# Optimization experiments

Measured on AMD Instinct MI355X. Metric: run time of the kernel, lower is better.

The kernel has to match this reference:

```python
import jax, jax.numpy as jnp
import numpy as np

B, T, D_MODEL, H, W = 2, 3, 32, 256, 256
N_HEADS, N_LEVELS, N_POINTS = 4, 3, 4


def conv2d(x, w, b, padding=1, dilation=1):
    y = jax.lax.conv_general_dilated(
        x, w, window_strides=(1, 1),
        padding=[(padding, padding), (padding, padding)],
        rhs_dilation=(dilation, dilation),
        dimension_numbers=('NCHW', 'OIHW', 'NCHW'))
    return y + b[None, :, None, None]


def lrelu(x):
    return jnp.where(x >= 0, x, 0.1 * x)


def bilinear_sample(img, x, y):
    # img: (N,C,H,W); x,y: (N,H',W') pixel coords; zero padding outside (grid_sample zeros)
    N, C, Hh, Ww = img.shape
    x0 = jnp.floor(x); y0 = jnp.floor(y)
    lx = x - x0; ly = y - y0
    imf = img.reshape(N, C, Hh * Ww)
    out = jnp.zeros((N, C) + x.shape[1:], img.dtype)
    for dy, dx, wgt in ((0, 0, (1 - lx) * (1 - ly)), (0, 1, lx * (1 - ly)),
                        (1, 0, (1 - lx) * ly), (1, 1, lx * ly)):
        xi = x0 + dx; yi = y0 + dy
        valid = (xi >= 0) & (xi < Ww) & (yi >= 0) & (yi < Hh)
        idx = (jnp.clip(yi, 0, Hh - 1) * Ww + jnp.clip(xi, 0, Ww - 1)).astype(jnp.int32)
        g = jnp.take_along_axis(imf, idx.reshape(N, 1, -1), axis=2).reshape((N, C) + x.shape[1:])
        out = out + g * (wgt * valid)[:, None]
    return out


def flow_warp(x, flow):
    # torch flow_warp with align_corners=True == sampling at pixel coords grid+flow
    N, C, Hh, Ww = x.shape
    gy, gx = jnp.meshgrid(jnp.arange(Hh, dtype=x.dtype), jnp.arange(Ww, dtype=x.dtype), indexing='ij')
    return bilinear_sample(x, gx[None] + flow[:, 0], gy[None] + flow[:, 1])


def ms_deform_attn(value, sampling_locations, attention_weights, h, w):
    # value: (N, L*h*w, Hh, d); loc: (N, Lq, Hh, L, P, 2) in [0,1]; weights: (N, Lq, Hh, L, P)
    # Matches MSDA CUDA kernel: sample at loc*(W,H)-0.5, bilinear, zero pad outside.
    N, _, Hh, d = value.shape
    Lq = sampling_locations.shape[1]
    L, P = sampling_locations.shape[3], sampling_locations.shape[4]
    out = jnp.zeros((N, Lq, Hh, d), value.dtype)
    for l in range(L):
        v = value[:, l * h * w:(l + 1) * h * w].transpose(0, 2, 1, 3)  # (N,Hh,hw,d)
        loc = sampling_locations[:, :, :, l]  # (N,Lq,Hh,P,2)
        x = loc[..., 0] * w - 0.5
        y = loc[..., 1] * h - 0.5
        x0 = jnp.floor(x); y0 = jnp.floor(y)
        lx = x - x0; ly = y - y0
        samp = jnp.zeros((N, Lq, Hh, P, d), value.dtype)
        for dy, dx, wgt in ((0, 0, (1 - lx) * (1 - ly)), (0, 1, lx * (1 - ly)),
                            (1, 0, (1 - lx) * ly), (1, 1, lx * ly)):
            xi = x0 + dx; yi = y0 + dy
            valid = (xi >= 0) & (xi < w) & (yi >= 0) & (yi < h)
            idx = (jnp.clip(yi, 0, h - 1) * w + jnp.clip(xi, 0, w - 1)).astype(jnp.int32)
            idx = idx.transpose(0, 2, 1, 3).reshape(N, Hh, Lq * P)
            g = jnp.take_along_axis(v, idx[..., None], axis=2)  # (N,Hh,Lq*P,d)
            g = g.reshape(N, Hh, Lq, P, d).transpose(0, 2, 1, 3, 4)
            samp = samp + g * (wgt * valid)[..., None]
        out = out + (samp * attention_weights[:, :, :, l][..., None]).sum(axis=3)
    return out.reshape(N, Lq, Hh * d)


def setup_inputs() -> dict:
    key = jax.random.key(0)
    ks = jax.random.split(key, 24)
    def rn(k, shape, s=1.0):
        return jax.random.normal(k, shape, dtype=jnp.float32) * s
    c = D_MODEL
    nofp = N_HEADS * N_LEVELS * N_POINTS
    return {
        'frame': rn(ks[0], (B, T, c, H, W)),
        'srcframe': rn(ks[1], (B, T, c, H, W)),
        'flow_forward': rn(ks[2], (B, T - 1, 2, H, W), 2.0),
        'flow_backward': rn(ks[3], (B, T - 1, 2, H, W), 2.0),
        'W_qk': rn(ks[4], (3 * c, 3 * c + 4, 3, 3), 0.05), 'b_qk': rn(ks[5], (3 * c,), 0.05),
        'W_v': rn(ks[6], (3 * c, 3 * c, 3, 3), 0.05), 'b_v': rn(ks[7], (3 * c,), 0.05),
        'W_vp': rn(ks[8], (c, c, 3, 3), 0.05), 'b_vp': rn(ks[9], (c,), 0.05),
        'W_off': rn(ks[10], (nofp * 2, 3 * c, 3, 3), 0.01), 'b_off': rn(ks[11], (nofp * 2,), 0.5),
        'W_aw': rn(ks[12], (nofp, 3 * c, 3, 3), 0.05), 'b_aw': rn(ks[13], (nofp,), 0.05),
        'W_out': rn(ks[14], (c, c, 3, 3), 0.05), 'b_out': rn(ks[15], (c,), 0.05),
        'W_ffd': rn(ks[16], (c, c, 3, 3), 0.05), 'b_ffd': rn(ks[17], (c,), 0.05),
        'W_ff1': rn(ks[18], (c, 2 * c, 3, 3), 0.05), 'b_ff1': rn(ks[19], (c,), 0.05),
        'W_ff2': rn(ks[20], (c, c, 3, 3), 0.05), 'b_ff2': rn(ks[21], (c,), 0.05),
        'W_fu': rn(ks[22], (c, c, 1, 1), 0.05), 'b_fu': rn(ks[23], (c,), 0.05),
    }


def reference(frame, srcframe, flow_forward, flow_backward,
              W_qk, b_qk, W_v, b_v, W_vp, b_vp, W_off, b_off, W_aw, b_aw,
              W_out, b_out, W_ffd, b_ffd, W_ff1, b_ff1, W_ff2, b_ff2, W_fu, b_fu):
    b, t, c, h, w = frame.shape
    Hh, L, P = N_HEADS, N_LEVELS, N_POINTS
    d = c // Hh
    # flow-warped neighbor frames + flows -> query embedding
    warp01 = flow_warp(frame[:, 0], flow_backward[:, 0])
    warp21 = flow_warp(frame[:, 2], flow_forward[:, 1])
    qk_in = jnp.concatenate([warp01, frame[:, 1], warp21,
                             flow_forward[:, 1], flow_backward[:, 0]], axis=1)
    qureys = lrelu(conv2d(qk_in, W_qk, b_qk))                       # (b, 3c, h, w)
    value = conv2d(frame.reshape(b, t * c, h, w), W_v, b_v)         # (b, 3c, h, w)
    # --- MSDeformAttn_Fusion ---
    val = conv2d(value.reshape(b * t, c, h, w), W_vp, b_vp).reshape(b, t, c, h, w)
    off = conv2d(qureys, W_off, b_off)                               # (b, Hh*L*P*2, h, w)
    aw = conv2d(qureys, W_aw, b_aw)                                  # (b, Hh*L*P, h, w)
    value_flat = val.reshape(b, t, c, h * w).transpose(0, 1, 3, 2).reshape(b, t * h * w, Hh, d)
    off = off.reshape(b, -1, h * w).transpose(0, 2, 1).reshape(b, h * w, Hh, L, P, 2)
    aw = aw.reshape(b, -1, h * w).transpose(0, 2, 1).reshape(b, h * w, Hh, L * P)
    aw = jax.nn.softmax(aw, axis=-1).reshape(b, h * w, Hh, L, P)
    # reference points: pixel centers normalized (masks all zero -> valid_ratios == 1)
    gy, gx = jnp.meshgrid((jnp.arange(h, dtype=off.dtype) + 0.5) / h,
                          (jnp.arange(w, dtype=off.dtype) + 0.5) / w, indexing='ij')
    ref = jnp.stack([gx.reshape(-1), gy.reshape(-1)], -1)            # (hw, 2) (x, y)
    normalizer = jnp.array([w, h], dtype=off.dtype)                  # same for all levels
    loc = ref[None, :, None, None, None, :] + off / normalizer
    attn_out = ms_deform_attn(value_flat, loc, aw, h, w)             # (b, hw, c)
    out = attn_out.reshape(b, h, w, c).transpose(0, 3, 1, 2)
    out = conv2d(out, W_out, b_out)                                  # output_proj
    # --- post-attention ---
    out = conv2d(out, W_ffd, b_ffd) + frame[:, 1]
    tseq = jnp.concatenate([out, srcframe[:, 1]], axis=1)            # (b, 2c, h, w)
    ff = conv2d(lrelu(conv2d(tseq, W_ff1, b_ff1, padding=2, dilation=2)), W_ff2, b_ff2)
    out = out + ff
    out = lrelu(conv2d(out, W_fu, b_fu, padding=0))                  # fusion 1x1
    return out
```

## Files before the change

kernel.cpp:

```cpp
#include <hip/hip_runtime.h>
#include <hip/hip_bf16.h>

typedef __hip_bfloat16 bf16;
typedef unsigned short us;
typedef unsigned int u32;
typedef __attribute__((ext_vector_type(8))) short short8;
typedef __attribute__((ext_vector_type(8))) unsigned short ushortx8;
typedef __attribute__((ext_vector_type(2))) float f32x2;
typedef __attribute__((ext_vector_type(4))) float f32x4;
typedef __attribute__((ext_vector_type(16))) float f32x16;

#define HW 65536
#define IMW 256
#define IMH 256

static __device__ __forceinline__ float u2f(us u) {
  return __uint_as_float(((unsigned)u) << 16);
}
static __device__ __forceinline__ us f2bu(float x) {
  bf16 h = __float2bfloat16(x);
  return *reinterpret_cast<us*>(&h);
}
static __device__ __forceinline__ unsigned pk2(float a, float b) {
  return (unsigned)f2bu(a) | ((unsigned)f2bu(b) << 16);
}

static __device__ __forceinline__ void gload_lds16(const void* g, void* l) {
  __builtin_amdgcn_global_load_lds(
      (const __attribute__((address_space(1))) u32*)g,
      (__attribute__((address_space(3))) u32*)l, 16, 0, 0);
}

struct PrepArgs {
  const float* src[9];
  us* dst[9];
  int OC[9], CIN[9], KPAD[9], LAY[9];
};

__global__ __launch_bounds__(256) void prep_weights(PrepArgs a) {
  int j = blockIdx.y;
  int n = blockIdx.x * 256 + threadIdx.x;
  int OC = a.OC[j], CIN = a.CIN[j], KPAD = a.KPAD[j];
  int tot = 9 * OC * KPAD;
  if (n >= tot) return;
  int oc, k;
  if (a.LAY[j] == 0) {
    int G = OC >> 4, NKC = KPAD >> 5;
    int e = n & 7;
    int m = (n >> 3) & 15;
    int q = (n >> 7) & 3;
    int rest = n >> 9;
    int kc = rest % NKC;
    int tg = rest / NKC;
    int g = tg % G;
    int t = tg / G;
    oc = g * 16 + m;
    k = kc * 32 + q * 8 + e;
    float v = (k < CIN) ? a.src[j][(size_t)(oc * CIN + k) * 9 + t] : 0.f;
    a.dst[j][n] = f2bu(v);
  } else {
    int OCT = OC >> 5, KH = KPAD >> 4;
    int e = n & 7;
    int l = (n >> 3) & 63;
    int rest = n >> 9;
    int jt = rest % OCT;
    int u = rest / OCT;
    int kh = u % KH;
    int t = u / KH;
    oc = jt * 32 + (l & 31);
    k = kh * 16 + (l >> 5) * 8 + e;
    float v = (k < CIN) ? a.src[j][(size_t)(oc * CIN + k) * 9 + t] : 0.f;
    a.dst[j][n] = f2bu(v);
  }
}

__global__ __launch_bounds__(256) void frame_to_nhwc(const float* __restrict__ frame,
                                                     unsigned* __restrict__ fn) {
  int pix = blockIdx.x * 256 + threadIdx.x;
  int b = blockIdx.y;
  const float* s = frame + (size_t)b * 96 * HW + pix;
  unsigned u[48];
#pragma unroll
  for (int j = 0; j < 48; ++j)
    u[j] = pk2(s[(size_t)(2 * j) * HW], s[(size_t)(2 * j + 1) * HW]);
  unsigned* d = fn + ((size_t)b * HW + pix) * 48;
#pragma unroll
  for (int j = 0; j < 12; ++j) {
    uint4 w;
    w.x = u[4 * j]; w.y = u[4 * j + 1]; w.z = u[4 * j + 2]; w.w = u[4 * j + 3];
    *(uint4*)&d[4 * j] = w;
  }
}

static __device__ void warp_nhwc(const us* __restrict__ fn, size_t bbase, int coff,
                                 float x, float y, unsigned* uo) {
  float x0f = floorf(x), y0f = floorf(y);
  float lx = x - x0f, ly = y - y0f;
  int x0 = (int)x0f, y0 = (int)y0f;
  float wt[4] = {(1.f - lx) * (1.f - ly), lx * (1.f - ly), (1.f - lx) * ly, lx * ly};
  float acc[32] = {};
#pragma unroll
  for (int k = 0; k < 4; ++k) {
    int xi = x0 + (k & 1), yi = y0 + (k >> 1);
    if ((unsigned)xi < IMW && (unsigned)yi < IMH) {
      const ushortx8* s =
          (const ushortx8*)(fn + (bbase + (size_t)yi * IMW + xi) * 96 + coff);
      float w = wt[k];
#pragma unroll
      for (int cj = 0; cj < 4; ++cj) {
        ushortx8 vv = s[cj];
#pragma unroll
        for (int e = 0; e < 8; ++e)
          acc[cj * 8 + e] = fmaf(w, u2f(vv[e]), acc[cj * 8 + e]);
      }
    }
  }
#pragma unroll
  for (int j = 0; j < 16; ++j) uo[j] = pk2(acc[2 * j], acc[2 * j + 1]);
}

__global__ __launch_bounds__(256) void build_qkin(
    const us* __restrict__ fn, const float* __restrict__ flowf,
    const float* __restrict__ flowb, unsigned* __restrict__ qk) {
  int pix = blockIdx.x * 256 + threadIdx.x;
  int b = blockIdx.y;
  int px = pix & 255, py = pix >> 8;

  float fbx = flowb[((size_t)(b * 2 + 0) * 2 + 0) * HW + pix];
  float fby = flowb[((size_t)(b * 2 + 0) * 2 + 1) * HW + pix];
  float ffx = flowf[((size_t)(b * 2 + 1) * 2 + 0) * HW + pix];
  float ffy = flowf[((size_t)(b * 2 + 1) * 2 + 1) * HW + pix];

  unsigned u[50];
  {
    const unsigned* s = (const unsigned*)(fn + ((size_t)b * HW + pix) * 96);
#pragma unroll
    for (int j = 0; j < 16; ++j) u[16 + j] = s[16 + j];
  }
  u[48] = pk2(ffx, ffy);
  u[49] = pk2(fbx, fby);

  warp_nhwc(fn, (size_t)b * HW, 0, (float)px + fbx, (float)py + fby, &u[0]);
  warp_nhwc(fn, (size_t)b * HW, 64, (float)px + ffx, (float)py + ffy, &u[32]);

  unsigned* qb = qk + ((size_t)b * HW + pix) * 50;
#pragma unroll
  for (int j = 0; j < 25; ++j) {
    uint2 t;
    t.x = u[2 * j];
    t.y = u[2 * j + 1];
    *(uint2*)(qb + 2 * j) = t;
  }
}

template <int CIN, int CST, int KPAD, int OCT, int KHC, bool LRELU>
__global__ __launch_bounds__(256) void conv3x3_m32(
    const us* __restrict__ in, const us* __restrict__ W2,
    const float* __restrict__ bias, us* __restrict__ out, int out_cst,
    int out_coff) {
  constexpr int COLS = 18, ROWS = 10, HALO = COLS * ROWS;
  constexpr int CIPAD = KPAD + 8;
  constexpr int CH = KPAD / 8;
  constexpr int KH = KPAD / 16;
  constexpr int SPT = KH / KHC;
  constexpr int NSTG = 9 * SPT;
  constexpr int CHB = KHC * OCT;
  __shared__ alignas(16) short lds[HALO * CIPAD];
  __shared__ alignas(16) short wlds[2][CHB * 512];

  const int z = blockIdx.z;
  const int px0 = blockIdx.x * 16, py0 = blockIdx.y * 8;
  const int lane = threadIdx.x & 63;
  const int wv = threadIdx.x >> 6;
  const int n = lane & 31;
  const int sr = n >> 4;
  const int colp = n & 15;
  const int kq = lane >> 5;

  f32x16 acc[OCT];
#pragma unroll
  for (int j = 0; j < OCT; ++j) acc[j] = 0.f;

  for (int c = threadIdx.x; c < HALO * CH; c += 256) {
    int p = c / CH, cb = c - p * CH;
    int row = p / COLS, col = p - row * COLS;
    int gy = py0 + row - 1, gx = px0 + col - 1;
    bool ok = ((unsigned)gy < IMH) && ((unsigned)gx < IMW);
    int ci0 = cb * 8;
    const us* gp = in + ((size_t)z * HW + (size_t)gy * IMW + gx) * CST + ci0;
    if (CIN == KPAD) {
      short8 v = (short8)0;
      if (ok) v = *(const short8*)gp;
      *(short8*)&lds[p * CIPAD + ci0] = v;
    } else {
      uint2 h0; h0.x = 0; h0.y = 0;
      uint2 h1; h1.x = 0; h1.y = 0;
      if (ok && ci0 + 4 <= CIN) h0 = *(const uint2*)gp;
      if (ok && ci0 + 8 <= CIN) h1 = *(const uint2*)(gp + 4);
      *(uint2*)&lds[p * CIPAD + ci0] = h0;
      *(uint2*)&lds[p * CIPAD + ci0 + 4] = h1;
    }
  }

#pragma unroll
  for (int r = 0; r < (CHB + 3) / 4; ++r) {
    int blk = r * 4 + wv;
    if (blk < CHB)
      gload_lds16(W2 + (size_t)(blk * 64 + lane) * 8, &wlds[0][blk * 512]);
  }
  __syncthreads();

  const int lanebase = ((wv * 2 + sr) * COLS + colp) * CIPAD + kq * 8;

  int buf = 0;
#pragma unroll 1
  for (int s = 0; s < NSTG; ++s) {
    if (s + 1 < NSTG) {
      const us* wn = W2 + (size_t)(s + 1) * (CHB * 512);
#pragma unroll
      for (int r = 0; r < (CHB + 3) / 4; ++r) {
        int blk = r * 4 + wv;
        if (blk < CHB)
          gload_lds16(wn + (size_t)(blk * 64 + lane) * 8,
                      &wlds[buf ^ 1][blk * 512]);
      }
    }
    const int t = s / SPT;
    const int kh0 = (s - t * SPT) * KHC;
    const int dy = t / 3 - 1, dx = t - (t / 3) * 3 - 1;
    const int sb = lanebase + ((dy + 1) * COLS + (dx + 1)) * CIPAD + kh0 * 16;
#pragma unroll
    for (int khr = 0; khr < KHC; ++khr) {
      short8 bf = *(const short8*)&lds[sb + khr * 16];
#pragma unroll
      for (int j = 0; j < OCT; ++j) {
        short8 af =
            *(const short8*)&wlds[buf][(khr * OCT + j) * 512 + lane * 8];
        acc[j] =
            __builtin_amdgcn_mfma_f32_32x32x16_bf16(af, bf, acc[j], 0, 0, 0);
      }
    }
    __syncthreads();
    buf ^= 1;
  }

  {
    int row = py0 + wv * 2 + sr;
    int pxc = px0 + colp;
    us* ob = out + ((size_t)z * HW + (size_t)row * IMW + pxc) * out_cst + out_coff;
#pragma unroll
    for (int j = 0; j < OCT; ++j) {
#pragma unroll
      for (int hi = 0; hi < 4; ++hi) {
        int oc0 = j * 32 + hi * 8 + kq * 4;
        f32x4 bb = *(const f32x4*)&bias[oc0];
        float v0 = acc[j][4 * hi + 0] + bb[0];
        float v1 = acc[j][4 * hi + 1] + bb[1];
        float v2 = acc[j][4 * hi + 2] + bb[2];
        float v3 = acc[j][4 * hi + 3] + bb[3];
        if (LRELU) {
          v0 = v0 >= 0.f ? v0 : 0.1f * v0;
          v1 = v1 >= 0.f ? v1 : 0.1f * v1;
          v2 = v2 >= 0.f ? v2 : 0.1f * v2;
          v3 = v3 >= 0.f ? v3 : 0.1f * v3;
        }
        uint2 w;
        w.x = pk2(v0, v1);
        w.y = pk2(v2, v3);
        *(uint2*)&ob[oc0] = w;
      }
    }
  }
}

template <int CIN, int CST, int KPAD, int DIL, int G, int ZDIV, int CSUB,
          int RES, int OUTMODE, bool LRELU>
__global__ __launch_bounds__(256) void conv3x3_mfma(
    const us* __restrict__ in, const us* __restrict__ W2,
    const float* __restrict__ bias, void* __restrict__ out, int out_cst,
    int out_coff, float* __restrict__ outB, const float* __restrict__ res,
    int res_cst, int res_coff) {
  constexpr int OC = G * 16;
  constexpr int COLS = 16 + 2 * DIL;
  constexpr int ROWS = 8 + 2 * DIL;
  constexpr int HALO = ROWS * COLS;
  constexpr int CIPAD = KPAD + 8;
  constexpr int CH = KPAD / 8;
  constexpr int NKC = KPAD / 32;
  constexpr int GW0 = (G + 1) / 2;
  constexpr int NU = 9 * NKC;
  __shared__ alignas(16) short lds[HALO * CIPAD];

  const int z = blockIdx.z;
  const int bin = z / ZDIV;
  const int coff = (z % ZDIV) * CSUB;
  const int px0 = blockIdx.x * 16, py0 = blockIdx.y * 8;
  const int lane = threadIdx.x & 63;
  const int wv = threadIdx.x >> 6;
  const int m = lane & 15, q = lane >> 4;
  const int gh = wv & 1, rh = wv >> 1;
  const int goff = gh * GW0;

  f32x4 acc[GW0][4];
#pragma unroll
  for (int g = 0; g < GW0; ++g)
#pragma unroll
    for (int r = 0; r < 4; ++r) acc[g][r] = 0.f;

  for (int c = threadIdx.x; c < HALO * CH; c += 256) {
    int p = c / CH, cb = c - p * CH;
    int row = p / COLS, col = p - row * COLS;
    int gy = py0 + row - DIL, gx = px0 + col - DIL;
    bool ok = ((unsigned)gy < IMH) && ((unsigned)gx < IMW);
    int ci0 = cb * 8;
    const us* gp = in + ((size_t)bin * HW + (size_t)gy * IMW + gx) * CST + coff + ci0;
    if (CIN == KPAD) {
      short8 v = (short8)0;
      if (ok) v = *(const short8*)gp;
      *(short8*)&lds[p * CIPAD + ci0] = v;
    } else {
      uint2 h0; h0.x = 0; h0.y = 0;
      uint2 h1; h1.x = 0; h1.y = 0;
      if (ok && ci0 + 4 <= CIN) h0 = *(const uint2*)gp;
      if (ok && ci0 + 8 <= CIN) h1 = *(const uint2*)(gp + 4);
      *(uint2*)&lds[p * CIPAD + ci0] = h0;
      *(uint2*)&lds[p * CIPAD + ci0 + 4] = h1;
    }
  }
  __syncthreads();

  const us* wl = W2 + (size_t)lane * 8;
  short8 af[2][GW0];
#pragma unroll
  for (int g = 0; g < GW0; ++g)
    if (goff + g < G)
      af[0][g] = *(const short8*)(wl + (size_t)((goff + g) * NKC) * 512);

#pragma unroll
  for (int u = 0; u < NU; ++u) {
    const int t = u / NKC, kc = u - t * NKC;
    if (u + 1 < NU) {
      const int t1 = (u + 1) / NKC, kc1 = (u + 1) - t1 * NKC;
#pragma unroll
      for (int g = 0; g < GW0; ++g)
        if (goff + g < G)
          af[(u + 1) & 1][g] =
              *(const short8*)(wl + (size_t)((t1 * G + goff + g) * NKC + kc1) * 512);
    }
    const int dy = t / 3 - 1, dx = t - (t / 3) * 3 - 1;
    short8 bfr[4];
#pragma unroll
    for (int r = 0; r < 4; ++r) {
      int rr = rh * 4 + r + DIL + dy * DIL;
      int cc = m + DIL + dx * DIL;
      bfr[r] = *(const short8*)&lds[(rr * COLS + cc) * CIPAD + kc * 32 + q * 8];
    }
#pragma unroll
    for (int g = 0; g < GW0; ++g)
      if (goff + g < G)
#pragma unroll
        for (int r = 0; r < 4; ++r)
          acc[g][r] = __builtin_amdgcn_mfma_f32_16x16x32_bf16(af[u & 1][g], bfr[r],
                                                              acc[g][r], 0, 0, 0);
  }

#pragma unroll
  for (int g = 0; g < GW0; ++g) {
    if (goff + g < G) {
      int oc0 = (goff + g) * 16 + q * 4;
      f32x4 bb = *(const f32x4*)&bias[oc0];
#pragma unroll
      for (int r = 0; r < 4; ++r) {
        int py = py0 + rh * 4 + r;
        int px = px0 + m;
        size_t pix = (size_t)py * IMW + px;
        f32x4 v;
#pragma unroll
        for (int e = 0; e < 4; ++e) {
          float x = acc[g][r][e] + bb[e];
          if (LRELU) x = x >= 0.f ? x : 0.1f * x;
          v[e] = x;
        }
        if (RES == 1) {
          f32x4 rv = *(const f32x4*)&res[((size_t)z * HW + pix) * res_cst + oc0];
#pragma unroll
          for (int e = 0; e < 4; ++e) v[e] += rv[e];
        }
        if (RES == 2) {
#pragma unroll
          for (int e = 0; e < 4; ++e)
            v[e] += res[((size_t)z * res_cst + res_coff + oc0 + e) * HW + pix];
        }
        if (OUTMODE == 0 || OUTMODE == 3) {
          uint2 w;
          w.x = pk2(v[0], v[1]);
          w.y = pk2(v[2], v[3]);
          *(uint2*)&((us*)out)[((size_t)z * HW + pix) * out_cst + out_coff + oc0] = w;
        }
        if (OUTMODE == 2)
          *(f32x4*)&((float*)out)[((size_t)z * HW + pix) * out_cst + oc0] = v;
        if (OUTMODE == 3)
          *(f32x4*)&outB[((size_t)z * HW + pix) * 32 + oc0] = v;
      }
    }
  }
}

__global__ __launch_bounds__(256) void deform_attn(
    const us* __restrict__ valp, const us* __restrict__ off,
    const float* __restrict__ aw, us* __restrict__ outp) {
  int tid = threadIdx.x;
  int half = tid & 1;
  int hh = (tid >> 1) & 3;
  int pix = blockIdx.x * 32 + (tid >> 3);
  int b = blockIdx.y;
  int px = pix & (IMW - 1), py = pix >> 8;

  us os[12];
  {
    const uint2* ob = (const uint2*)(off + ((size_t)b * HW + pix) * 96 +
                                     hh * 24 + half * 12);
    uint2 a0 = ob[0], a1 = ob[1], a2 = ob[2];
    *(uint2*)&os[0] = a0;
    *(uint2*)&os[4] = a1;
    *(uint2*)&os[8] = a2;
  }
  float wv[6];
  {
    const f32x2* ab = (const f32x2*)(aw + ((size_t)b * HW + pix) * 48 +
                                     hh * 12 + half * 6);
    f32x2 a0 = ab[0], a1 = ab[1], a2 = ab[2];
    wv[0] = a0.x; wv[1] = a0.y; wv[2] = a1.x;
    wv[3] = a1.y; wv[4] = a2.x; wv[5] = a2.y;
  }

  float m6 = wv[0];
#pragma unroll
  for (int i = 1; i < 6; ++i) m6 = fmaxf(m6, wv[i]);
  float mx = fmaxf(m6, __shfl_xor(m6, 1));
  float s6 = 0.f;
#pragma unroll
  for (int i = 0; i < 6; ++i) {
    wv[i] = __expf(wv[i] - mx);
    s6 += wv[i];
  }
  float inv = 1.f / (s6 + __shfl_xor(s6, 1));

  f32x2 acc2[4];
#pragma unroll
  for (int j = 0; j < 4; ++j) acc2[j] = 0.f;

#pragma unroll
  for (int i = 0; i < 6; ++i) {
    int pp = half * 6 + i;
    int l = pp >> 2;
    const us* vbase = valp + ((size_t)(b * 3 + l) * HW) * 32 + hh * 8;
    float x = (float)px + u2f(os[2 * i]);
    float y = (float)py + u2f(os[2 * i + 1]);
    float x0f = floorf(x), y0f = floorf(y);
    float lx = x - x0f, ly = y - y0f;
    int x0 = (int)x0f, y0 = (int)y0f;
    bool vx0 = (unsigned)x0 < IMW, vx1 = (unsigned)(x0 + 1) < IMW;
    bool vy0 = (unsigned)y0 < IMH, vy1 = (unsigned)(y0 + 1) < IMH;
    float a = wv[i] * inv;
    float ax0 = (1.f - lx) * a, ax1 = lx * a;
    float w00 = ax0 * (1.f - ly), w01 = ax1 * (1.f - ly);
    float w10 = ax0 * ly, w11 = ax1 * ly;
    const us* p00 = vbase + (size_t)((long)(y0 * IMW + x0)) * 32;
#pragma unroll
    for (int c = 0; c < 4; ++c) {
      bool ok = (c & 1 ? vx1 : vx0) && (c & 2 ? vy1 : vy0);
      float w = (c == 0) ? w00 : (c == 1) ? w01 : (c == 2) ? w10 : w11;
      const us* p = p00 + (c & 1) * 32 + (c >> 1) * (IMW * 32);
      if (ok) {
        uint4 uu = *(const uint4*)p;
        unsigned uarr[4] = {uu.x, uu.y, uu.z, uu.w};
#pragma unroll
        for (int j = 0; j < 4; ++j) {
          f32x2 v;
          v.x = __uint_as_float(uarr[j] << 16);
          v.y = __uint_as_float(uarr[j] & 0xffff0000u);
          acc2[j] += v * w;
        }
      }
    }
  }

  float accf[8];
#pragma unroll
  for (int j = 0; j < 4; ++j) {
    accf[2 * j] = acc2[j].x + __shfl_xor(acc2[j].x, 1);
    accf[2 * j + 1] = acc2[j].y + __shfl_xor(acc2[j].y, 1);
  }
  if (half == 0) {
    ushortx8 sv;
#pragma unroll
    for (int dd = 0; dd < 8; ++dd) sv[dd] = f2bu(accf[dd]);
    *(ushortx8*)(outp + ((size_t)b * HW + pix) * 32 + hh * 8) = sv;
  }
}

__global__ __launch_bounds__(256) void copy_src(const float* __restrict__ src,
                                                unsigned* __restrict__ out1b) {
  int pix = blockIdx.x * 256 + threadIdx.x;
  int b = blockIdx.y;
  const float* s = src + ((size_t)(b * 3 + 1) * 32) * HW + pix;
  unsigned u[16];
#pragma unroll
  for (int j = 0; j < 16; ++j)
    u[j] = pk2(s[(size_t)(2 * j) * HW], s[(size_t)(2 * j + 1) * HW]);
  unsigned* d = out1b + ((size_t)b * HW + pix) * 32 + 16;
#pragma unroll
  for (int j = 0; j < 4; ++j) {
    uint4 w;
    w.x = u[4 * j]; w.y = u[4 * j + 1]; w.z = u[4 * j + 2]; w.w = u[4 * j + 3];
    *(uint4*)&d[4 * j] = w;
  }
}

__global__ __launch_bounds__(256) void conv1x1_fu(
    const float* __restrict__ in, const float* __restrict__ wgt,
    const float* __restrict__ bias, float* __restrict__ out) {
  int pix = blockIdx.x * 256 + threadIdx.x;
  int b = blockIdx.y;
  float vin[32];
  {
    const f32x4* s = (const f32x4*)(in + ((size_t)b * HW + pix) * 32);
#pragma unroll
    for (int j = 0; j < 8; ++j) {
      f32x4 v = s[j];
#pragma unroll
      for (int e = 0; e < 4; ++e) vin[4 * j + e] = v[e];
    }
  }
#pragma unroll 1
  for (int oc = 0; oc < 32; ++oc) {
    float a = bias[oc];
#pragma unroll
    for (int ci = 0; ci < 32; ++ci) a = fmaf(wgt[oc * 32 + ci], vin[ci], a);
    a = a >= 0.f ? a : 0.1f * a;
    out[((size_t)b * 32 + oc) * HW + pix] = a;
  }
}

extern "C" void kernel_launch(void* const* d_in, const int* in_sizes, int n_in,
                              void* d_out, int out_size, void* d_ws, size_t ws_size,
                              hipStream_t stream) {
  (void)in_sizes; (void)n_in; (void)out_size;
  if (ws_size < 25614592ull * 4) return;

  const float* frame = (const float*)d_in[0];
  const float* srcframe = (const float*)d_in[1];
  const float* flowf = (const float*)d_in[2];
  const float* flowb = (const float*)d_in[3];

  float* ws = (float*)d_ws;
  us* wsu = (us*)d_ws;

  static const int w2off[9] = {0,      110592, 193536, 202752, 285696,
                               327168, 336384, 345600, 364032};
  us* fnhwc = (us*)(ws + 186624);
  unsigned* qk_u = (unsigned*)(ws + 6478080);
  us* qk = (us*)qk_u;
  us* Q = (us*)(ws + 13031680);
  us* V = (us*)(ws + 6478080);
  us* Vp = (us*)(ws + 19323136);
  us* offb = (us*)(ws + 186624);
  float* awb = (float*)(ws + 6478080);
  us* attn = (us*)(ws + 13031680);
  us* convout = (us*)(ws + 13031680 + 2097152);
  us* out1b = (us*)(ws + 6478080);
  unsigned* out1b_u = (unsigned*)out1b;
  float* out1f = (float*)(ws + 19323136);
  us* ff1out = (us*)(ws + 186624);
  float* out2 = (float*)(ws + 13031680);

  {
    PrepArgs pa;
    static const int srcidx[9] = {4, 6, 8, 10, 12, 14, 16, 18, 20};
    static const int OCs[9] = {96, 96, 32, 96, 48, 32, 32, 32, 32};
    static const int CINs[9] = {100, 96, 32, 96, 96, 32, 32, 64, 32};
    static const int KPADs[9] = {128, 96, 32, 96, 96, 32, 32, 64, 32};
    static const int LAYs[9] = {1, 1, 0, 1, 0, 0, 0, 0, 0};
    for (int i = 0; i < 9; ++i) {
      pa.src[i] = (const float*)d_in[srcidx[i]];
      pa.dst[i] = wsu + w2off[i];
      pa.OC[i] = OCs[i];
      pa.CIN[i] = CINs[i];
      pa.KPAD[i] = KPADs[i];
      pa.LAY[i] = LAYs[i];
    }
    prep_weights<<<dim3(432, 9), 256, 0, stream>>>(pa);
  }

  frame_to_nhwc<<<dim3(256, 2), 256, 0, stream>>>(frame, (unsigned*)fnhwc);

  build_qkin<<<dim3(256, 2), 256, 0, stream>>>(fnhwc, flowf, flowb, qk_u);

  dim3 cg2(16, 32, 2);

  conv3x3_m32<100, 100, 128, 3, 4, true><<<cg2, 256, 0, stream>>>(
      qk, wsu + w2off[0], (const float*)d_in[5], Q, 96, 0);

  conv3x3_m32<96, 96, 96, 3, 6, false><<<cg2, 256, 0, stream>>>(
      fnhwc, wsu + w2off[1], (const float*)d_in[7], V, 96, 0);

  conv3x3_mfma<32, 96, 32, 1, 2, 3, 32, 0, 0, false><<<dim3(16, 32, 6), 256, 0, stream>>>(
      V, wsu + w2off[2], (const float*)d_in[9], Vp, 32, 0, nullptr, nullptr, 0, 0);

  conv3x3_m32<96, 96, 96, 3, 6, false><<<cg2, 256, 0, stream>>>(
      Q, wsu + w2off[3], (const float*)d_in[11], offb, 96, 0);

  conv3x3_mfma<96, 96, 96, 1, 3, 1, 0, 0, 2, false><<<cg2, 256, 0, stream>>>(
      Q, wsu + w2off[4], (const float*)d_in[13], awb, 48, 0, nullptr, nullptr, 0, 0);

  deform_attn<<<dim3(2048, 2), 256, 0, stream>>>(Vp, offb, awb, attn);

  conv3x3_mfma<32, 32, 32, 1, 2, 1, 0, 0, 0, false><<<cg2, 256, 0, stream>>>(
      attn, wsu + w2off[5], (const float*)d_in[15], convout, 32, 0, nullptr, nullptr, 0, 0);

  conv3x3_mfma<32, 32, 32, 1, 2, 1, 0, 2, 3, false><<<cg2, 256, 0, stream>>>(
      convout, wsu + w2off[6], (const float*)d_in[17], out1b, 64, 0, out1f, frame, 96, 32);

  copy_src<<<dim3(256, 2), 256, 0, stream>>>(srcframe, out1b_u);

  conv3x3_mfma<64, 64, 64, 2, 2, 1, 0, 0, 0, true><<<cg2, 256, 0, stream>>>(
      out1b, wsu + w2off[7], (const float*)d_in[19], ff1out, 32, 0, nullptr, nullptr, 0, 0);

  conv3x3_mfma<32, 32, 32, 1, 2, 1, 0, 1, 2, false><<<cg2, 256, 0, stream>>>(
      ff1out, wsu + w2off[8], (const float*)d_in[21], out2, 32, 0, nullptr, out1f, 32, 0);

  conv1x1_fu<<<dim3(256, 2), 256, 0, stream>>>(out2, (const float*)d_in[22],
                                               (const float*)d_in[23], (float*)d_out);
}
```

Before: 461.3 us.

## Widen m32 conv tiles to 32 columns and stream input channels in chunks

The 32x32 MFMA conv kernel now covers a 32x8 pixel tile per block, with each wave running two MFMA column fragments that share the same weight fragment. This halves weight LDS reads per output. The input channels are staged into LDS in 32-channel chunks instead of all at once, which keeps the wider halo within LDS limits. Weight prep is reordered to match the chunk-then-tap staging. The cost is half as many blocks, more accumulator registers, and an extra sync per chunk with no overlap between halo loads and compute.

```diff
diff --git a/kernel.cpp b/kernel.cpp
--- a/kernel.cpp
+++ b/kernel.cpp
@@ -34,7 +34,7 @@
 struct PrepArgs {
   const float* src[9];
   us* dst[9];
-  int OC[9], CIN[9], KPAD[9], LAY[9];
+  int OC[9], CIN[9], KPAD[9], LAY[9], KCH[9];
 };
 
 __global__ __launch_bounds__(256) void prep_weights(PrepArgs a) {
@@ -59,16 +59,20 @@
     float v = (k < CIN) ? a.src[j][(size_t)(oc * CIN + k) * 9 + t] : 0.f;
     a.dst[j][n] = f2bu(v);
   } else {
-    int OCT = OC >> 5, KH = KPAD >> 4;
+    int OCT = OC >> 5;
+    int KCH = a.KCH[j];
+    int KHH = KCH >> 4;
     int e = n & 7;
     int l = (n >> 3) & 63;
     int rest = n >> 9;
     int jt = rest % OCT;
     int u = rest / OCT;
-    int kh = u % KH;
-    int t = u / KH;
+    int khi = u % KHH;
+    int sg = u / KHH;
+    int kc = sg / 9;
     oc = jt * 32 + (l & 31);
-    k = kh * 16 + (l >> 5) * 8 + e;
+    k = kc * KCH + khi * 16 + (l >> 5) * 8 + e;
+    int t = sg - kc * 9;
     float v = (k < CIN) ? a.src[j][(size_t)(oc * CIN + k) * 9 + t] : 0.f;
     a.dst[j][n] = f2bu(v);
   }
@@ -153,23 +157,23 @@
   }
 }
 
-template <int CIN, int CST, int KPAD, int OCT, int KHC, bool LRELU>
+template <int CIN, int CST, int KPAD, int KCH, int OCT, bool LRELU>
 __global__ __launch_bounds__(256) void conv3x3_m32(
     const us* __restrict__ in, const us* __restrict__ W2,
     const float* __restrict__ bias, us* __restrict__ out, int out_cst,
     int out_coff) {
-  constexpr int COLS = 18, ROWS = 10, HALO = COLS * ROWS;
-  constexpr int CIPAD = KPAD + 8;
-  constexpr int CH = KPAD / 8;
-  constexpr int KH = KPAD / 16;
-  constexpr int SPT = KH / KHC;
-  constexpr int NSTG = 9 * SPT;
-  constexpr int CHB = KHC * OCT;
+  constexpr int COLS = 34, ROWS = 10, HALO = COLS * ROWS;
+  constexpr int CIPAD = KCH + 8;
+  constexpr int CHc = KCH / 8;
+  constexpr int KHH = KCH / 16;
+  constexpr int NCH = KPAD / KCH;
+  constexpr int NSTG = NCH * 9;
+  constexpr int CHB = KHH * OCT;
   __shared__ alignas(16) short lds[HALO * CIPAD];
   __shared__ alignas(16) short wlds[2][CHB * 512];
 
   const int z = blockIdx.z;
-  const int px0 = blockIdx.x * 16, py0 = blockIdx.y * 8;
+  const int px0 = blockIdx.x * 32, py0 = blockIdx.y * 8;
   const int lane = threadIdx.x & 63;
   const int wv = threadIdx.x >> 6;
   const int n = lane & 31;
@@ -177,97 +181,111 @@
   const int colp = n & 15;
   const int kq = lane >> 5;
 
-  f32x16 acc[OCT];
-#pragma unroll
-  for (int j = 0; j < OCT; ++j) acc[j] = 0.f;
-
-  for (int c = threadIdx.x; c < HALO * CH; c += 256) {
-    int p = c / CH, cb = c - p * CH;
-    int row = p / COLS, col = p - row * COLS;
-    int gy = py0 + row - 1, gx = px0 + col - 1;
-    bool ok = ((unsigned)gy < IMH) && ((unsigned)gx < IMW);
-    int ci0 = cb * 8;
-    const us* gp = in + ((size_t)z * HW + (size_t)gy * IMW + gx) * CST + ci0;
-    if (CIN == KPAD) {
-      short8 v = (short8)0;
-      if (ok) v = *(const short8*)gp;
-      *(short8*)&lds[p * CIPAD + ci0] = v;
-    } else {
-      uint2 h0; h0.x = 0; h0.y = 0;
-      uint2 h1; h1.x = 0; h1.y = 0;
-      if (ok && ci0 + 4 <= CIN) h0 = *(const uint2*)gp;
-      if (ok && ci0 + 8 <= CIN) h1 = *(const uint2*)(gp + 4);
-      *(uint2*)&lds[p * CIPAD + ci0] = h0;
-      *(uint2*)&lds[p * CIPAD + ci0 + 4] = h1;
-    }
-  }
-
-#pragma unroll
-  for (int r = 0; r < (CHB + 3) / 4; ++r) {
-    int blk = r * 4 + wv;
-    if (blk < CHB)
-      gload_lds16(W2 + (size_t)(blk * 64 + lane) * 8, &wlds[0][blk * 512]);
-  }
-  __syncthreads();
-
-  const int lanebase = ((wv * 2 + sr) * COLS + colp) * CIPAD + kq * 8;
-
-  int buf = 0;
+  f32x16 acc[2][OCT];
+#pragma unroll
+  for (int f = 0; f < 2; ++f)
+#pragma unroll
+    for (int j = 0; j < OCT; ++j) acc[f][j] = 0.f;
+
+  const int rb = 2 * wv + sr;
+  const int base0 = ((rb + 1) * COLS + colp + 1) * CIPAD + kq * 8;
+  const int base1 = base0 + 16 * CIPAD;
+
+  int buf = 0, sg = 0;
 #pragma unroll 1
-  for (int s = 0; s < NSTG; ++s) {
-    if (s + 1 < NSTG) {
-      const us* wn = W2 + (size_t)(s + 1) * (CHB * 512);
+  for (int kc = 0; kc < NCH; ++kc) {
+    for (int c = threadIdx.x; c < HALO * CHc; c += 256) {
+      int p = c / CHc, cb = c - p * CHc;
+      int row = p / COLS, col = p - row * COLS;
+      int gy = py0 + row - 1, gx = px0 + col - 1;
+      bool ok = ((unsigned)gy < IMH) && ((unsigned)gx < IMW);
+      int cil = cb * 8;
+      int cig = kc * KCH + cil;
+      const us* gp = in + ((size_t)z * HW + (size_t)gy * IMW + gx) * CST + cig;
+      if (CIN == KPAD) {
+        short8 v = (short8)0;
+        if (ok) v = *(const short8*)gp;
+        *(short8*)&lds[p * CIPAD + cil] = v;
+      } else {
+        uint2 h0; h0.x = 0; h0.y = 0;
+        uint2 h1; h1.x = 0; h1.y = 0;
+        if (ok && cig + 4 <= CIN) h0 = *(const uint2*)gp;
+        if (ok && cig + 8 <= CIN) h1 = *(const uint2*)(gp + 4);
+        *(uint2*)&lds[p * CIPAD + cil] = h0;
+        *(uint2*)&lds[p * CIPAD + cil + 4] = h1;
+      }
+    }
+    if (kc == 0) {
 #pragma unroll
       for (int r = 0; r < (CHB + 3) / 4; ++r) {
         int blk = r * 4 + wv;
         if (blk < CHB)
-          gload_lds16(wn + (size_t)(blk * 64 + lane) * 8,
-                      &wlds[buf ^ 1][blk * 512]);
-      }
-    }
-    const int t = s / SPT;
-    const int kh0 = (s - t * SPT) * KHC;
-    const int dy = t / 3 - 1, dx = t - (t / 3) * 3 - 1;
-    const int sb = lanebase + ((dy + 1) * COLS + (dx + 1)) * CIPAD + kh0 * 16;
-#pragma unroll
-    for (int khr = 0; khr < KHC; ++khr) {
-      short8 bf = *(const short8*)&lds[sb + khr * 16];
+          gload_lds16(W2 + (size_t)(blk * 64 + lane) * 8, &wlds[0][blk * 512]);
+      }
+    }
+    __syncthreads();
+
+#pragma unroll 1
+    for (int t = 0; t < 9; ++t, ++sg) {
+      if (sg + 1 < NSTG) {
+        const us* wn = W2 + (size_t)(sg + 1) * (CHB * 512);
+#pragma unroll
+        for (int r = 0; r < (CHB + 3) / 4; ++r) {
+          int blk = r * 4 + wv;
+          if (blk < CHB)
+            gload_lds16(wn + (size_t)(blk * 64 + lane) * 8,
+                        &wlds[buf ^ 1][blk * 512]);
+        }
+      }
+      const int dy = t / 3 - 1, dx = t - (t / 3) * 3 - 1;
+      const int toff = (dy * COLS + dx) * CIPAD;
+#pragma unroll
+      for (int khr = 0; khr < KHH; ++khr) {
+        short8 bf0 = *(const short8*)&lds[base0 + toff + khr * 16];
+        short8 bf1 = *(const short8*)&lds[base1 + toff + khr * 16];
+#pragma unroll
+        for (int j = 0; j < OCT; ++j) {
+          short8 af =
+              *(const short8*)&wlds[buf][(khr * OCT + j) * 512 + lane * 8];
+          acc[0][j] = __builtin_amdgcn_mfma_f32_32x32x16_bf16(af, bf0,
+                                                              acc[0][j], 0, 0, 0);
+          acc[1][j] = __builtin_amdgcn_mfma_f32_32x32x16_bf16(af, bf1,
+                                                              acc[1][j], 0, 0, 0);
+        }
+      }
+      __syncthreads();
+      buf ^= 1;
+    }
+  }
+
+  {
+    int row = py0 + rb;
+#pragma unroll
+    for (int f = 0; f < 2; ++f) {
+      int pxc = px0 + 16 * f + colp;
+      us* ob =
+          out + ((size_t)z * HW + (size_t)row * IMW + pxc) * out_cst + out_coff;
 #pragma unroll
       for (int j = 0; j < OCT; ++j) {
-        short8 af =
-            *(const short8*)&wlds[buf][(khr * OCT + j) * 512 + lane * 8];
-        acc[j] =
-            __builtin_amdgcn_mfma_f32_32x32x16_bf16(af, bf, acc[j], 0, 0, 0);
-      }
-    }
-    __syncthreads();
-    buf ^= 1;
-  }
-
-  {
-    int row = py0 + wv * 2 + sr;
-    int pxc = px0 + colp;
-    us* ob = out + ((size_t)z * HW + (size_t)row * IMW + pxc) * out_cst + out_coff;
-#pragma unroll
-    for (int j = 0; j < OCT; ++j) {
-#pragma unroll
-      for (int hi = 0; hi < 4; ++hi) {
-        int oc0 = j * 32 + hi * 8 + kq * 4;
-        f32x4 bb = *(const f32x4*)&bias[oc0];
-        float v0 = acc[j][4 * hi + 0] + bb[0];
-        float v1 = acc[j][4 * hi + 1] + bb[1];
-        float v2 = acc[j][4 * hi + 2] + bb[2];
-        float v3 = acc[j][4 * hi + 3] + bb[3];
-        if (LRELU) {
-          v0 = v0 >= 0.f ? v0 : 0.1f * v0;
-          v1 = v1 >= 0.f ? v1 : 0.1f * v1;
-          v2 = v2 >= 0.f ? v2 : 0.1f * v2;
-          v3 = v3 >= 0.f ? v3 : 0.1f * v3;
-        }
-        uint2 w;
-        w.x = pk2(v0, v1);
-        w.y = pk2(v2, v3);
-        *(uint2*)&ob[oc0] = w;
+#pragma unroll
+        for (int hi = 0; hi < 4; ++hi) {
+          int oc0 = j * 32 + hi * 8 + kq * 4;
+          f32x4 bb = *(const f32x4*)&bias[oc0];
+          float v0 = acc[f][j][4 * hi + 0] + bb[0];
+          float v1 = acc[f][j][4 * hi + 1] + bb[1];
+          float v2 = acc[f][j][4 * hi + 2] + bb[2];
+          float v3 = acc[f][j][4 * hi + 3] + bb[3];
+          if (LRELU) {
+            v0 = v0 >= 0.f ? v0 : 0.1f * v0;
+            v1 = v1 >= 0.f ? v1 : 0.1f * v1;
+            v2 = v2 >= 0.f ? v2 : 0.1f * v2;
+            v3 = v3 >= 0.f ? v3 : 0.1f * v3;
+          }
+          uint2 w;
+          w.x = pk2(v0, v1);
+          w.y = pk2(v2, v3);
+          *(uint2*)&ob[oc0] = w;
+        }
       }
     }
   }
@@ -582,6 +600,7 @@
     static const int CINs[9] = {100, 96, 32, 96, 96, 32, 32, 64, 32};
     static const int KPADs[9] = {128, 96, 32, 96, 96, 32, 32, 64, 32};
     static const int LAYs[9] = {1, 1, 0, 1, 0, 0, 0, 0, 0};
+    static const int KCHs[9] = {32, 32, 32, 32, 32, 32, 32, 32, 32};
     for (int i = 0; i < 9; ++i) {
       pa.src[i] = (const float*)d_in[srcidx[i]];
       pa.dst[i] = wsu + w2off[i];
@@ -589,6 +608,7 @@
       pa.CIN[i] = CINs[i];
       pa.KPAD[i] = KPADs[i];
       pa.LAY[i] = LAYs[i];
+      pa.KCH[i] = KCHs[i];
     }
     prep_weights<<<dim3(432, 9), 256, 0, stream>>>(pa);
   }
@@ -598,17 +618,18 @@
   build_qkin<<<dim3(256, 2), 256, 0, stream>>>(fnhwc, flowf, flowb, qk_u);
 
   dim3 cg2(16, 32, 2);
-
-  conv3x3_m32<100, 100, 128, 3, 4, true><<<cg2, 256, 0, stream>>>(
+  dim3 cg32(8, 32, 2);
+
+  conv3x3_m32<100, 100, 128, 32, 3, true><<<cg32, 256, 0, stream>>>(
       qk, wsu + w2off[0], (const float*)d_in[5], Q, 96, 0);
 
-  conv3x3_m32<96, 96, 96, 3, 6, false><<<cg2, 256, 0, stream>>>(
+  conv3x3_m32<96, 96, 96, 32, 3, false><<<cg32, 256, 0, stream>>>(
       fnhwc, wsu + w2off[1], (const float*)d_in[7], V, 96, 0);
 
   conv3x3_mfma<32, 96, 32, 1, 2, 3, 32, 0, 0, false><<<dim3(16, 32, 6), 256, 0, stream>>>(
       V, wsu + w2off[2], (const float*)d_in[9], Vp, 32, 0, nullptr, nullptr, 0, 0);
 
-  conv3x3_m32<96, 96, 96, 3, 6, false><<<cg2, 256, 0, stream>>>(
+  conv3x3_m32<96, 96, 96, 32, 3, false><<<cg32, 256, 0, stream>>>(
       Q, wsu + w2off[3], (const float*)d_in[11], offb, 96, 0);
 
   conv3x3_mfma<96, 96, 96, 1, 3, 1, 0, 0, 2, false><<<cg2, 256, 0, stream>>>(
```

New measurement: 460.5 us. About the same (-0.2%).
